# Kernel tuning notes

Measured on AMD Instinct MI355X. Metric: run time of the kernel, lower is better.

The kernel has to match this reference:

```python
import jax, jax.numpy as jnp
import numpy as np

T, D, DFF, E, K = 2048, 1024, 2816, 8, 2


def setup_inputs() -> dict:
    key = jax.random.key(0)
    k1, k2, k3, k4, k5, k6 = jax.random.split(key, 6)
    return {
        "x": jax.random.normal(k1, (T, D), dtype=jnp.float32),
        "topk_weight": jax.random.uniform(k2, (T, K), dtype=jnp.float32),
        "gate_w": jax.random.normal(k3, (E, DFF, D), dtype=jnp.float32) * 0.02,
        "up_w": jax.random.normal(k4, (E, DFF, D), dtype=jnp.float32) * 0.02,
        "down_w": jax.random.normal(k5, (E, D, DFF), dtype=jnp.float32) * 0.02,
        "topk_ids": jax.random.randint(k6, (T, K), 0, E, dtype=jnp.int64),
    }


def reference(x, topk_weight, gate_w, up_w, down_w, topk_ids):
    # x: [T, D]; topk_ids/topk_weight: [T, K]
    # Per expert: SwiGLU MLP over all tokens, combined with the per-token
    # routing weight for that expert (0 if the expert was not selected).
    out = jnp.zeros_like(x)
    num_experts = gate_w.shape[0]
    for e in range(num_experts):
        h = jax.nn.silu(x @ gate_w[e].T) * (x @ up_w[e].T)  # [T, DFF]
        y = h @ down_w[e].T                                  # [T, D]
        # sum over top-k slots of routing weight where this expert was chosen
        w_e = jnp.sum(jnp.where(topk_ids == e, topk_weight, 0.0), axis=1)  # [T]
        out = out + y * w_e[:, None]
    return out
```

## Files before the change

### kernel.cpp

```cpp
#include <hip/hip_runtime.h>
#include <stdint.h>

typedef __attribute__((ext_vector_type(8))) __bf16 bf16x8;
typedef __attribute__((ext_vector_type(4))) float f32x4;
typedef __attribute__((ext_vector_type(8))) unsigned short ushort8;

#define T_TOK 2048
#define D_DIM 1024
#define DFF   2816
#define NEXP  8
#define NROWS 4096
#define BK    32
#define NW_ELEM (NEXP * DFF * D_DIM)
#define MAXTM2 24

#define SWZ(r,g) ((g) ^ (((r) >> 1) & 3))

#define TL_N    0
#define TL_BASE 16
#define TL_VAL  80
#define TL_EXP  144

__device__ __forceinline__ void lds_cp16(const void* g, void* l) {
  __builtin_amdgcn_global_load_lds(
      (const __attribute__((address_space(1))) void*)g,
      (__attribute__((address_space(3))) void*)l, 16, 0, 0);
}

__device__ __forceinline__ ushort8 pack_bf16x8(float4 a, float4 b) {
  union { __bf16 h[8]; ushort8 u; } r;
  r.h[0] = (__bf16)a.x; r.h[1] = (__bf16)a.y; r.h[2] = (__bf16)a.z; r.h[3] = (__bf16)a.w;
  r.h[4] = (__bf16)b.x; r.h[5] = (__bf16)b.y; r.h[6] = (__bf16)b.z; r.h[7] = (__bf16)b.w;
  return r.u;
}

__device__ __forceinline__ unsigned short f2bf(float f) {
  union { __bf16 h; unsigned short u; } r;
  r.h = (__bf16)f;
  return r.u;
}

__device__ __forceinline__ float bf2f(unsigned short u) {
  union { uint32_t u; float f; } v; v.u = (uint32_t)u << 16;
  return v.f;
}

#define PIPE_BARRIER_VM3() do { \
    asm volatile("s_waitcnt vmcnt(3)" ::: "memory"); \
    __builtin_amdgcn_s_barrier(); \
  } while (0)

__global__ __launch_bounds__(512) void routing_kernel(
    const int* __restrict__ ids, const float* __restrict__ w,
    int* __restrict__ cnt, int* __restrict__ off,
    int* __restrict__ tok, float* __restrict__ wgt, int* __restrict__ rowmap,
    int* __restrict__ tl2)
{
  __shared__ int s_cnt[NEXP];
  __shared__ int s_off[NEXP];
  const int lane = threadIdx.x & 63;
  const int e    = threadIdx.x >> 6;

  int total = 0;
  for (int c = 0; c < NROWS / 64; ++c) {
    int id = ids[c * 64 + lane];
    unsigned long long b = __ballot(id == e);
    total += __popcll(b);
  }
  if (lane == 0) s_cnt[e] = total;
  __syncthreads();
  if (threadIdx.x == 0) {
    int acc = 0, n2 = 0;
    for (int i = 0; i < NEXP; ++i) {
      s_off[i] = acc; off[i] = acc; cnt[i] = s_cnt[i];
      for (int j = 0; j < s_cnt[i]; j += 256) {
        tl2[TL_BASE + n2] = acc + j;
        tl2[TL_VAL  + n2] = min(256, s_cnt[i] - j);
        tl2[TL_EXP  + n2] = i;
        ++n2;
      }
      acc += s_cnt[i];
    }
    tl2[TL_N] = n2;
  }
  __syncthreads();
  int base = s_off[e];
  for (int c = 0; c < NROWS / 64; ++c) {
    int idx = c * 64 + lane;
    int id = ids[idx];
    bool m = (id == e);
    unsigned long long b = __ballot(m);
    int pos = __popcll(b & ((1ull << lane) - 1ull));
    if (m) {
      tok[base + pos] = idx >> 1;
      wgt[base + pos] = w[idx];
      rowmap[idx] = base + pos;
    }
    base += __popcll(b);
  }
}

__global__ __launch_bounds__(256) void gather_x_kernel(
    const float* __restrict__ x, const int* __restrict__ tok,
    unsigned short* __restrict__ xg)
{
  const int i = blockIdx.x;
  const int t = tok[i];
  const float4 v = ((const float4*)(x + (size_t)t * D_DIM))[threadIdx.x];
  ushort4 o;
  o.x = f2bf(v.x); o.y = f2bf(v.y); o.z = f2bf(v.z); o.w = f2bf(v.w);
  ((ushort4*)(xg + (size_t)i * D_DIM))[threadIdx.x] = o;
}

__global__ __launch_bounds__(256) void wconv_gu_kernel(
    const float* __restrict__ gw, const float* __restrict__ uw,
    unsigned short* __restrict__ gb, unsigned short* __restrict__ ub)
{
  const size_t n = NW_ELEM / 8;
  const size_t stride = (size_t)gridDim.x * blockDim.x;
  for (size_t i = (size_t)blockIdx.x * blockDim.x + threadIdx.x;
       i < 2 * n; i += stride) {
    const bool up = (i >= n);
    const size_t idx = (up ? i - n : i) * 8;
    const float* src = up ? uw : gw;
    unsigned short* dst = up ? ub : gb;
    float4 a = *(const float4*)(src + idx);
    float4 b = *(const float4*)(src + idx + 4);
    *(ushort8*)(dst + idx) = pack_bf16x8(a, b);
  }
}

#define BM_A 256
#define BN_A 64
#define NT_A (DFF / BN_A)
#define NWORK_A (MAXTM2 * NT_A)
#define WCD_BLKS 1024
#define NWG_A (NWORK_A + WCD_BLKS)
#define KT_A (D_DIM / BK)

__global__ __launch_bounds__(512) void moe_gateup_bf(
    const unsigned short* __restrict__ gbuf, const unsigned short* __restrict__ ubuf,
    const unsigned short* __restrict__ xg, const float* __restrict__ wgt,
    const int* __restrict__ tl2,
    unsigned short* __restrict__ hbuf,
    const float* __restrict__ down_w, unsigned short* __restrict__ dbuf)
{
  const int bid = blockIdx.x;
  const int ntm = tl2[TL_N];
  const int nwork = ntm * NT_A;
  const int tid = threadIdx.x;
  if (bid >= nwork) {
    if (bid >= NWORK_A) {
      const int c = bid - NWORK_A;
      const size_t stride = (size_t)WCD_BLKS * 512;
      for (size_t i = (size_t)c * 512 + tid; i < NW_ELEM / 8; i += stride) {
        const size_t idx = i * 8;
        float4 a = *(const float4*)(down_w + idx);
        float4 b = *(const float4*)(down_w + idx + 4);
        *(ushort8*)(dbuf + idx) = pack_bf16x8(a, b);
      }
    }
    return;
  }
  const int tile = bid % ntm;
  const int nt   = bid / ntm;
  const int row_base = tl2[TL_BASE + tile];
  const int valid    = tl2[TL_VAL  + tile];
  const int e        = tl2[TL_EXP  + tile];
  const int n0 = nt * BN_A;

  __shared__ __align__(16) unsigned short Alds[3][BM_A * BK];
  __shared__ __align__(16) unsigned short Bg[3][BN_A * BK];
  __shared__ __align__(16) unsigned short Bu[3][BN_A * BK];

  const int lane = tid & 63;
  const int wid = tid >> 6;
  const int wm = wid >> 1, wn = wid & 1;
  const int lhi = lane >> 4, llo = lane & 15;

  f32x4 accg[4][2], accu[4][2];
  #pragma unroll
  for (int i = 0; i < 4; ++i)
    #pragma unroll
    for (int j = 0; j < 2; ++j) {
      accg[i][j] = (f32x4){0.f, 0.f, 0.f, 0.f};
      accu[i][j] = (f32x4){0.f, 0.f, 0.f, 0.f};
    }

  const unsigned short* gb = gbuf + ((size_t)e * DFF + n0) * D_DIM;
  const unsigned short* ub = ubuf + ((size_t)e * DFF + n0) * D_DIM;

  const int ar0 = tid >> 2, ag = tid & 3;
  const int ar1 = ar0 + 128;
  const size_t a_src0 = (size_t)(row_base + min(ar0, valid - 1)) * D_DIM + SWZ(ar0, ag) * 8;
  const size_t a_src1 = (size_t)(row_base + min(ar1, valid - 1)) * D_DIM + SWZ(ar1, ag) * 8;
  const int q = tid & 255;
  const int br = q >> 2, bg2 = q & 3;
  const size_t b_src = (size_t)br * D_DIM + SWZ(br, bg2) * 8;
  const unsigned short* bsrc_base = (tid < 256) ? gb : ub;
  unsigned short* bdst[3];
  bdst[0] = (tid < 256) ? &Bg[0][q * 8] : &Bu[0][q * 8];
  bdst[1] = (tid < 256) ? &Bg[1][q * 8] : &Bu[1][q * 8];
  bdst[2] = (tid < 256) ? &Bg[2][q * 8] : &Bu[2][q * 8];

  lds_cp16(xg + a_src0, &Alds[0][tid * 8]);
  lds_cp16(xg + a_src1, &Alds[0][(tid + 512) * 8]);
  lds_cp16(bsrc_base + b_src, bdst[0]);
  {
    const int k1 = BK;
    lds_cp16(xg + a_src0 + k1, &Alds[1][tid * 8]);
    lds_cp16(xg + a_src1 + k1, &Alds[1][(tid + 512) * 8]);
    lds_cp16(bsrc_base + b_src + k1, bdst[1]);
  }

  int cur = 0;
  for (int t = 0; t < KT_A; ++t) {
    PIPE_BARRIER_VM3();

    const int nb = (cur + 2 >= 3) ? cur - 1 : cur + 2;
    const int kn = (t + 2 < KT_A) ? (t + 2) * BK : 0;
    lds_cp16(xg + a_src0 + kn, &Alds[nb][tid * 8]);
    lds_cp16(xg + a_src1 + kn, &Alds[nb][(tid + 512) * 8]);
    lds_cp16(bsrc_base + b_src + kn, bdst[nb]);

    bf16x8 a[4], bgf[2], buf_[2];
    #pragma unroll
    for (int mi = 0; mi < 4; ++mi) {
      int row = wm * 64 + mi * 16 + llo;
      a[mi] = *(const bf16x8*)&Alds[cur][row * BK + SWZ(row, lhi) * 8];
    }
    #pragma unroll
    for (int ni = 0; ni < 2; ++ni) {
      int row = wn * 32 + ni * 16 + llo;
      bgf[ni]  = *(const bf16x8*)&Bg[cur][row * BK + SWZ(row, lhi) * 8];
      buf_[ni] = *(const bf16x8*)&Bu[cur][row * BK + SWZ(row, lhi) * 8];
    }
    #pragma unroll
    for (int mi = 0; mi < 4; ++mi)
      #pragma unroll
      for (int ni = 0; ni < 2; ++ni) {
        accg[mi][ni] = __builtin_amdgcn_mfma_f32_16x16x32_bf16(a[mi], bgf[ni], accg[mi][ni], 0, 0, 0);
        accu[mi][ni] = __builtin_amdgcn_mfma_f32_16x16x32_bf16(a[mi], buf_[ni], accu[mi][ni], 0, 0, 0);
      }

    cur = (cur + 1 >= 3) ? 0 : cur + 1;
  }

  #pragma unroll
  for (int mi = 0; mi < 4; ++mi) {
    #pragma unroll
    for (int r = 0; r < 4; ++r) {
      int row = wm * 64 + mi * 16 + lhi * 4 + r;
      if (row < valid) {
        int grow = row_base + row;
        float wv = wgt[grow];
        size_t base = (size_t)grow * DFF + n0 + wn * 32;
        #pragma unroll
        for (int ni = 0; ni < 2; ++ni) {
          float g = accg[mi][ni][r];
          float u = accu[mi][ni][r];
          float h = (g / (1.f + __expf(-g))) * u * wv;
          hbuf[base + ni * 16 + llo] = f2bf(h);
        }
      }
    }
  }
}

#define BM_B 256
#define BN_B 128
#define NT_B (D_DIM / BN_B)
#define SLICES_B 4
#define NWG_B (MAXTM2 * NT_B * SLICES_B)

template <bool USE_YBUF>
__global__ __launch_bounds__(512) void moe_down_bf(
    const unsigned short* __restrict__ dbuf,
    const unsigned short* __restrict__ hbuf,
    const int* __restrict__ tok,
    const int* __restrict__ tl2,
    unsigned short* __restrict__ ybuf, float* __restrict__ out_atomic)
{
  constexpr int KS = DFF / SLICES_B;
  constexpr int KT = KS / BK;

  const int bid = blockIdx.x;
  const int ntm = tl2[TL_N];
  const int nwork = ntm * NT_B * SLICES_B;
  if (bid >= nwork) return;
  const int tile = bid % ntm;
  const int r1_  = bid / ntm;
  const int nt = r1_ % NT_B;
  const int sl = r1_ / NT_B;
  const int row_base = tl2[TL_BASE + tile];
  const int valid    = tl2[TL_VAL  + tile];
  const int e        = tl2[TL_EXP  + tile];
  const int n0 = nt * BN_B;
  const int kbeg = sl * KS;

  __shared__ __align__(16) unsigned short Alds[3][BM_B * BK];
  __shared__ __align__(16) unsigned short Blds[3][BN_B * BK];

  const int tid = threadIdx.x, lane = tid & 63, wid = tid >> 6;
  const int wm = wid >> 1, wn = wid & 1;
  const int lhi = lane >> 4, llo = lane & 15;

  f32x4 acc[4][4];
  #pragma unroll
  for (int i = 0; i < 4; ++i)
    #pragma unroll
    for (int j = 0; j < 4; ++j) acc[i][j] = (f32x4){0.f, 0.f, 0.f, 0.f};

  const unsigned short* db = dbuf + ((size_t)e * D_DIM + n0) * DFF;

  const int ar0 = tid >> 2, ag = tid & 3;
  const int ar1 = ar0 + 128;
  const size_t a_src0 = (size_t)(row_base + min(ar0, valid - 1)) * DFF + SWZ(ar0, ag) * 8;
  const size_t a_src1 = (size_t)(row_base + min(ar1, valid - 1)) * DFF + SWZ(ar1, ag) * 8;
  const int brr = tid >> 2, bgg = tid & 3;
  const size_t b_src = (size_t)brr * DFF + SWZ(brr, bgg) * 8;

  lds_cp16(hbuf + a_src0 + kbeg, &Alds[0][tid * 8]);
  lds_cp16(hbuf + a_src1 + kbeg, &Alds[0][(tid + 512) * 8]);
  lds_cp16(db + b_src + kbeg, &Blds[0][tid * 8]);
  {
    const int k1 = kbeg + BK;
    lds_cp16(hbuf + a_src0 + k1, &Alds[1][tid * 8]);
    lds_cp16(hbuf + a_src1 + k1, &Alds[1][(tid + 512) * 8]);
    lds_cp16(db + b_src + k1, &Blds[1][tid * 8]);
  }

  int cur = 0;
  for (int t = 0; t < KT; ++t) {
    PIPE_BARRIER_VM3();

    const int nb = (cur + 2 >= 3) ? cur - 1 : cur + 2;
    const int kn = kbeg + ((t + 2 < KT) ? (t + 2) * BK : 0);
    lds_cp16(hbuf + a_src0 + kn, &Alds[nb][tid * 8]);
    lds_cp16(hbuf + a_src1 + kn, &Alds[nb][(tid + 512) * 8]);
    lds_cp16(db + b_src + kn, &Blds[nb][tid * 8]);

    bf16x8 a[4], b[4];
    #pragma unroll
    for (int mi = 0; mi < 4; ++mi) {
      int row = wm * 64 + mi * 16 + llo;
      a[mi] = *(const bf16x8*)&Alds[cur][row * BK + SWZ(row, lhi) * 8];
    }
    #pragma unroll
    for (int ni = 0; ni < 4; ++ni) {
      int row = wn * 64 + ni * 16 + llo;
      b[ni] = *(const bf16x8*)&Blds[cur][row * BK + SWZ(row, lhi) * 8];
    }
    #pragma unroll
    for (int mi = 0; mi < 4; ++mi)
      #pragma unroll
      for (int ni = 0; ni < 4; ++ni)
        acc[mi][ni] = __builtin_amdgcn_mfma_f32_16x16x32_bf16(a[mi], b[ni], acc[mi][ni], 0, 0, 0);

    cur = (cur + 1 >= 3) ? 0 : cur + 1;
  }

  #pragma unroll
  for (int mi = 0; mi < 4; ++mi) {
    #pragma unroll
    for (int r = 0; r < 4; ++r) {
      int row = wm * 64 + mi * 16 + lhi * 4 + r;
      if (row < valid) {
        if (USE_YBUF) {
          unsigned short* yp = ybuf + ((size_t)sl * NROWS + row_base + row) * D_DIM + n0 + wn * 64;
          #pragma unroll
          for (int ni = 0; ni < 4; ++ni) yp[ni * 16 + llo] = f2bf(acc[mi][ni][r]);
        } else {
          int tk = tok[row_base + row];
          float* op = out_atomic + (size_t)tk * D_DIM + n0 + wn * 64;
          #pragma unroll
          for (int ni = 0; ni < 4; ++ni) atomicAdd(op + ni * 16 + llo, acc[mi][ni][r]);
        }
      }
    }
  }
}

__global__ __launch_bounds__(256) void combine_kernel(
    const unsigned short* __restrict__ ybuf, const int* __restrict__ rowmap,
    float* __restrict__ out)
{
  const int t = blockIdx.x;
  const int d = threadIdx.x * 4;
  const int r0 = rowmap[t * 2], r1 = rowmap[t * 2 + 1];
  float s0 = 0.f, s1 = 0.f, s2 = 0.f, s3 = 0.f;
  #pragma unroll
  for (int sl = 0; sl < SLICES_B; ++sl) {
    ushort4 a = *(const ushort4*)(ybuf + ((size_t)sl * NROWS + r0) * D_DIM + d);
    ushort4 b = *(const ushort4*)(ybuf + ((size_t)sl * NROWS + r1) * D_DIM + d);
    s0 += bf2f(a.x) + bf2f(b.x);
    s1 += bf2f(a.y) + bf2f(b.y);
    s2 += bf2f(a.z) + bf2f(b.z);
    s3 += bf2f(a.w) + bf2f(b.w);
  }
  float4 s = {s0, s1, s2, s3};
  *(float4*)(out + (size_t)t * D_DIM + d) = s;
}

extern "C" void kernel_launch(void* const* d_in, const int* in_sizes, int n_in,
                              void* d_out, int out_size, void* d_ws, size_t ws_size,
                              hipStream_t stream) {
  const float* x      = (const float*)d_in[0];
  const float* topk_w = (const float*)d_in[1];
  const float* gate_w = (const float*)d_in[2];
  const float* up_w   = (const float*)d_in[3];
  const float* down_w = (const float*)d_in[4];
  const int*   ids    = (const int*)d_in[5];
  float* out = (float*)d_out;

  char* ws = (char*)d_ws;
  int*   cnt    = (int*)(ws + 0);
  int*   off    = (int*)(ws + 32);
  int*   tok    = (int*)(ws + 64);
  float* wgt    = (float*)(ws + 64 + NROWS * 4);
  int*   rowmap = (int*)(ws + 64 + NROWS * 8);
  int*   tl2    = (int*)(ws + 50688);

  const size_t XG_OFF = 65536;
  const size_t XG_SZ  = (size_t)NROWS * D_DIM * 2;
  const size_t HB_OFF = XG_OFF + XG_SZ;
  const size_t HB_SZ  = (size_t)NROWS * DFF * 2;
  const size_t W_SZ   = (size_t)NW_ELEM * 2;
  const size_t GB_OFF = HB_OFF + HB_SZ;
  const size_t UB_OFF = GB_OFF + W_SZ;
  const size_t DB_OFF = UB_OFF + W_SZ;
  const size_t YB_OFF = DB_OFF + W_SZ;
  const size_t YB_SZ  = (size_t)SLICES_B * NROWS * D_DIM * 2;

  unsigned short* xg   = (unsigned short*)(ws + XG_OFF);
  unsigned short* hbuf = (unsigned short*)(ws + HB_OFF);
  unsigned short* gbuf = (unsigned short*)(ws + GB_OFF);
  unsigned short* ubuf = (unsigned short*)(ws + UB_OFF);
  unsigned short* dbuf = (unsigned short*)(ws + DB_OFF);
  unsigned short* ybuf = (unsigned short*)(ws + YB_OFF);

  routing_kernel<<<1, 512, 0, stream>>>(ids, topk_w, cnt, off, tok, wgt, rowmap, tl2);
  gather_x_kernel<<<NROWS, 256, 0, stream>>>(x, tok, xg);
  wconv_gu_kernel<<<4096, 256, 0, stream>>>(gate_w, up_w, gbuf, ubuf);
  moe_gateup_bf<<<NWG_A, 512, 0, stream>>>(gbuf, ubuf, xg, wgt, tl2, hbuf, down_w, dbuf);

  if (ws_size >= YB_OFF + YB_SZ) {
    moe_down_bf<true><<<NWG_B, 512, 0, stream>>>(dbuf, hbuf, tok, tl2, ybuf, nullptr);
    combine_kernel<<<T_TOK, 256, 0, stream>>>(ybuf, rowmap, out);
  } else {
    hipMemsetAsync(d_out, 0, (size_t)out_size * sizeof(float), stream);
    moe_down_bf<false><<<NWG_B, 512, 0, stream>>>(dbuf, hbuf, tok, tl2, nullptr, out);
  }
}
```

Baseline: 242.3 us.

## Fuse gate/up weight conversion into panel-resident gate-up GEMM

Removes the separate fp32-to-bf16 conversion kernel for gate and up weights. Each block now loads a 32-column panel of gate and up weights straight from fp32, converts it into LDS once (about 128KB), and loops over all token tiles of its expert, streaming only activations through a double buffer. This avoids writing and re-reading bf16 weight copies in global memory. In exchange, LDS use per block is high, which limits occupancy, and the per-block panel load is not overlapped with compute.

```diff
diff --git a/kernel.cpp b/kernel.cpp
--- a/kernel.cpp
+++ b/kernel.cpp
@@ -44,11 +44,6 @@
   union { uint32_t u; float f; } v; v.u = (uint32_t)u << 16;
   return v.f;
 }
-
-#define PIPE_BARRIER_VM3() do { \
-    asm volatile("s_waitcnt vmcnt(3)" ::: "memory"); \
-    __builtin_amdgcn_s_barrier(); \
-  } while (0)
 
 __global__ __launch_bounds__(512) void routing_kernel(
     const int* __restrict__ ids, const float* __restrict__ w,
@@ -112,155 +107,131 @@
   ((ushort4*)(xg + (size_t)i * D_DIM))[threadIdx.x] = o;
 }
 
-__global__ __launch_bounds__(256) void wconv_gu_kernel(
-    const float* __restrict__ gw, const float* __restrict__ uw,
-    unsigned short* __restrict__ gb, unsigned short* __restrict__ ub)
-{
-  const size_t n = NW_ELEM / 8;
-  const size_t stride = (size_t)gridDim.x * blockDim.x;
-  for (size_t i = (size_t)blockIdx.x * blockDim.x + threadIdx.x;
-       i < 2 * n; i += stride) {
-    const bool up = (i >= n);
-    const size_t idx = (up ? i - n : i) * 8;
-    const float* src = up ? uw : gw;
-    unsigned short* dst = up ? ub : gb;
-    float4 a = *(const float4*)(src + idx);
-    float4 b = *(const float4*)(src + idx + 4);
-    *(ushort8*)(dst + idx) = pack_bf16x8(a, b);
-  }
-}
-
-#define BM_A 256
-#define BN_A 64
-#define NT_A (DFF / BN_A)
-#define NWORK_A (MAXTM2 * NT_A)
+#define BN_P 32
+#define NTP (DFF / BN_P)
+#define NWORK_P (NEXP * NTP)
 #define WCD_BLKS 1024
-#define NWG_A (NWORK_A + WCD_BLKS)
+#define NWG_P (NWORK_P + WCD_BLKS)
 #define KT_A (D_DIM / BK)
 
-__global__ __launch_bounds__(512) void moe_gateup_bf(
-    const unsigned short* __restrict__ gbuf, const unsigned short* __restrict__ ubuf,
+__global__ __launch_bounds__(512) void moe_gateup_panel(
+    const float* __restrict__ gate_w, const float* __restrict__ up_w,
     const unsigned short* __restrict__ xg, const float* __restrict__ wgt,
-    const int* __restrict__ tl2,
+    const int* __restrict__ cnt, const int* __restrict__ off,
     unsigned short* __restrict__ hbuf,
     const float* __restrict__ down_w, unsigned short* __restrict__ dbuf)
 {
   const int bid = blockIdx.x;
-  const int ntm = tl2[TL_N];
-  const int nwork = ntm * NT_A;
   const int tid = threadIdx.x;
-  if (bid >= nwork) {
-    if (bid >= NWORK_A) {
-      const int c = bid - NWORK_A;
-      const size_t stride = (size_t)WCD_BLKS * 512;
-      for (size_t i = (size_t)c * 512 + tid; i < NW_ELEM / 8; i += stride) {
-        const size_t idx = i * 8;
-        float4 a = *(const float4*)(down_w + idx);
-        float4 b = *(const float4*)(down_w + idx + 4);
-        *(ushort8*)(dbuf + idx) = pack_bf16x8(a, b);
-      }
+  if (bid >= NWORK_P) {
+    const int c = bid - NWORK_P;
+    const size_t stride = (size_t)WCD_BLKS * 512;
+    for (size_t i = (size_t)c * 512 + tid; i < NW_ELEM / 8; i += stride) {
+      const size_t idx = i * 8;
+      float4 a = *(const float4*)(down_w + idx);
+      float4 b = *(const float4*)(down_w + idx + 4);
+      *(ushort8*)(dbuf + idx) = pack_bf16x8(a, b);
     }
     return;
   }
-  const int tile = bid % ntm;
-  const int nt   = bid / ntm;
-  const int row_base = tl2[TL_BASE + tile];
-  const int valid    = tl2[TL_VAL  + tile];
-  const int e        = tl2[TL_EXP  + tile];
-  const int n0 = nt * BN_A;
-
-  __shared__ __align__(16) unsigned short Alds[3][BM_A * BK];
-  __shared__ __align__(16) unsigned short Bg[3][BN_A * BK];
-  __shared__ __align__(16) unsigned short Bu[3][BN_A * BK];
-
-  const int lane = tid & 63;
-  const int wid = tid >> 6;
-  const int wm = wid >> 1, wn = wid & 1;
+  const int e  = bid / NTP;
+  const int nt = bid % NTP;
+  const int cnte = cnt[e];
+  if (cnte == 0) return;
+  const int off_e = off[e];
+  const int n0 = nt * BN_P;
+
+  __shared__ __align__(16) unsigned short Bg[BN_P * D_DIM];
+  __shared__ __align__(16) unsigned short Bu[BN_P * D_DIM];
+  __shared__ __align__(16) unsigned short Alds[2][256 * BK];
+
+  {
+    const float* gp = gate_w + ((size_t)e * DFF + n0) * D_DIM;
+    const float* up = up_w   + ((size_t)e * DFF + n0) * D_DIM;
+    #pragma unroll
+    for (int it = 0; it < (BN_P * D_DIM / 8) / 512; ++it) {
+      const int c = it * 512 + tid;
+      const int r = c >> 7, g = c & 127;
+      const int dst = r * D_DIM + ((g ^ (r & 7)) * 8);
+      const float* s1 = gp + (size_t)r * D_DIM + g * 8;
+      *(ushort8*)&Bg[dst] = pack_bf16x8(*(const float4*)s1, *(const float4*)(s1 + 4));
+      const float* s2 = up + (size_t)r * D_DIM + g * 8;
+      *(ushort8*)&Bu[dst] = pack_bf16x8(*(const float4*)s2, *(const float4*)(s2 + 4));
+    }
+  }
+  __syncthreads();
+
+  const int lane = tid & 63, wid = tid >> 6;
   const int lhi = lane >> 4, llo = lane & 15;
-
-  f32x4 accg[4][2], accu[4][2];
-  #pragma unroll
-  for (int i = 0; i < 4; ++i)
-    #pragma unroll
-    for (int j = 0; j < 2; ++j) {
-      accg[i][j] = (f32x4){0.f, 0.f, 0.f, 0.f};
-      accu[i][j] = (f32x4){0.f, 0.f, 0.f, 0.f};
-    }
-
-  const unsigned short* gb = gbuf + ((size_t)e * DFF + n0) * D_DIM;
-  const unsigned short* ub = ubuf + ((size_t)e * DFF + n0) * D_DIM;
-
   const int ar0 = tid >> 2, ag = tid & 3;
   const int ar1 = ar0 + 128;
-  const size_t a_src0 = (size_t)(row_base + min(ar0, valid - 1)) * D_DIM + SWZ(ar0, ag) * 8;
-  const size_t a_src1 = (size_t)(row_base + min(ar1, valid - 1)) * D_DIM + SWZ(ar1, ag) * 8;
-  const int q = tid & 255;
-  const int br = q >> 2, bg2 = q & 3;
-  const size_t b_src = (size_t)br * D_DIM + SWZ(br, bg2) * 8;
-  const unsigned short* bsrc_base = (tid < 256) ? gb : ub;
-  unsigned short* bdst[3];
-  bdst[0] = (tid < 256) ? &Bg[0][q * 8] : &Bu[0][q * 8];
-  bdst[1] = (tid < 256) ? &Bg[1][q * 8] : &Bu[1][q * 8];
-  bdst[2] = (tid < 256) ? &Bg[2][q * 8] : &Bu[2][q * 8];
-
-  lds_cp16(xg + a_src0, &Alds[0][tid * 8]);
-  lds_cp16(xg + a_src1, &Alds[0][(tid + 512) * 8]);
-  lds_cp16(bsrc_base + b_src, bdst[0]);
-  {
-    const int k1 = BK;
-    lds_cp16(xg + a_src0 + k1, &Alds[1][tid * 8]);
-    lds_cp16(xg + a_src1 + k1, &Alds[1][(tid + 512) * 8]);
-    lds_cp16(bsrc_base + b_src + k1, bdst[1]);
-  }
-
-  int cur = 0;
-  for (int t = 0; t < KT_A; ++t) {
-    PIPE_BARRIER_VM3();
-
-    const int nb = (cur + 2 >= 3) ? cur - 1 : cur + 2;
-    const int kn = (t + 2 < KT_A) ? (t + 2) * BK : 0;
-    lds_cp16(xg + a_src0 + kn, &Alds[nb][tid * 8]);
-    lds_cp16(xg + a_src1 + kn, &Alds[nb][(tid + 512) * 8]);
-    lds_cp16(bsrc_base + b_src + kn, bdst[nb]);
-
-    bf16x8 a[4], bgf[2], buf_[2];
-    #pragma unroll
-    for (int mi = 0; mi < 4; ++mi) {
-      int row = wm * 64 + mi * 16 + llo;
-      a[mi] = *(const bf16x8*)&Alds[cur][row * BK + SWZ(row, lhi) * 8];
-    }
-    #pragma unroll
-    for (int ni = 0; ni < 2; ++ni) {
-      int row = wn * 32 + ni * 16 + llo;
-      bgf[ni]  = *(const bf16x8*)&Bg[cur][row * BK + SWZ(row, lhi) * 8];
-      buf_[ni] = *(const bf16x8*)&Bu[cur][row * BK + SWZ(row, lhi) * 8];
-    }
-    #pragma unroll
-    for (int mi = 0; mi < 4; ++mi)
+
+  const int nmt = (cnte + 255) >> 8;
+  for (int mt = 0; mt < nmt; ++mt) {
+    const int row_base = off_e + (mt << 8);
+    const int valid = min(256, cnte - (mt << 8));
+    const size_t a_src0 = (size_t)(row_base + min(ar0, valid - 1)) * D_DIM + SWZ(ar0, ag) * 8;
+    const size_t a_src1 = (size_t)(row_base + min(ar1, valid - 1)) * D_DIM + SWZ(ar1, ag) * 8;
+
+    f32x4 accg[2][2], accu[2][2];
+    #pragma unroll
+    for (int i = 0; i < 2; ++i)
+      #pragma unroll
+      for (int j = 0; j < 2; ++j) {
+        accg[i][j] = (f32x4){0.f, 0.f, 0.f, 0.f};
+        accu[i][j] = (f32x4){0.f, 0.f, 0.f, 0.f};
+      }
+
+    lds_cp16(xg + a_src0, &Alds[0][tid * 8]);
+    lds_cp16(xg + a_src1, &Alds[0][(tid + 512) * 8]);
+
+    for (int t = 0; t < KT_A; ++t) {
+      __builtin_amdgcn_s_barrier();
+      const int kn = (t + 1 < KT_A) ? (t + 1) * BK : 0;
+      lds_cp16(xg + a_src0 + kn, &Alds[(t + 1) & 1][tid * 8]);
+      lds_cp16(xg + a_src1 + kn, &Alds[(t + 1) & 1][(tid + 512) * 8]);
+      asm volatile("s_waitcnt vmcnt(2)" ::: "memory");
+      __builtin_amdgcn_s_barrier();
+
+      bf16x8 a[2], bgf[2], buf_[2];
+      #pragma unroll
+      for (int mi = 0; mi < 2; ++mi) {
+        int row = wid * 32 + mi * 16 + llo;
+        a[mi] = *(const bf16x8*)&Alds[t & 1][row * BK + SWZ(row, lhi) * 8];
+      }
       #pragma unroll
       for (int ni = 0; ni < 2; ++ni) {
-        accg[mi][ni] = __builtin_amdgcn_mfma_f32_16x16x32_bf16(a[mi], bgf[ni], accg[mi][ni], 0, 0, 0);
-        accu[mi][ni] = __builtin_amdgcn_mfma_f32_16x16x32_bf16(a[mi], buf_[ni], accu[mi][ni], 0, 0, 0);
-      }
-
-    cur = (cur + 1 >= 3) ? 0 : cur + 1;
-  }
-
-  #pragma unroll
-  for (int mi = 0; mi < 4; ++mi) {
-    #pragma unroll
-    for (int r = 0; r < 4; ++r) {
-      int row = wm * 64 + mi * 16 + lhi * 4 + r;
-      if (row < valid) {
-        int grow = row_base + row;
-        float wv = wgt[grow];
-        size_t base = (size_t)grow * DFF + n0 + wn * 32;
+        int rn = ni * 16 + llo;
+        int gk = t * 4 + lhi;
+        int eo = rn * D_DIM + ((gk ^ (rn & 7)) * 8);
+        bgf[ni]  = *(const bf16x8*)&Bg[eo];
+        buf_[ni] = *(const bf16x8*)&Bu[eo];
+      }
+      #pragma unroll
+      for (int mi = 0; mi < 2; ++mi)
         #pragma unroll
         for (int ni = 0; ni < 2; ++ni) {
-          float g = accg[mi][ni][r];
-          float u = accu[mi][ni][r];
-          float h = (g / (1.f + __expf(-g))) * u * wv;
-          hbuf[base + ni * 16 + llo] = f2bf(h);
+          accg[mi][ni] = __builtin_amdgcn_mfma_f32_16x16x32_bf16(a[mi], bgf[ni], accg[mi][ni], 0, 0, 0);
+          accu[mi][ni] = __builtin_amdgcn_mfma_f32_16x16x32_bf16(a[mi], buf_[ni], accu[mi][ni], 0, 0, 0);
+        }
+    }
+
+    #pragma unroll
+    for (int mi = 0; mi < 2; ++mi) {
+      #pragma unroll
+      for (int r_ = 0; r_ < 4; ++r_) {
+        int row = wid * 32 + mi * 16 + lhi * 4 + r_;
+        if (row < valid) {
+          int grow = row_base + row;
+          float wv = wgt[grow];
+          size_t base = (size_t)grow * DFF + n0;
+          #pragma unroll
+          for (int ni = 0; ni < 2; ++ni) {
+            float g = accg[mi][ni][r_];
+            float u = accu[mi][ni][r_];
+            float h = (g / (1.f + __expf(-g))) * u * wv;
+            hbuf[base + ni * 16 + llo] = f2bf(h);
+          }
         }
       }
     }
@@ -272,6 +243,11 @@
 #define NT_B (D_DIM / BN_B)
 #define SLICES_B 4
 #define NWG_B (MAXTM2 * NT_B * SLICES_B)
+
+#define PIPE_BARRIER_VM3() do { \
+    asm volatile("s_waitcnt vmcnt(3)" ::: "memory"); \
+    __builtin_amdgcn_s_barrier(); \
+  } while (0)
 
 template <bool USE_YBUF>
 __global__ __launch_bounds__(512) void moe_down_bf(
@@ -426,23 +402,19 @@
   const size_t HB_OFF = XG_OFF + XG_SZ;
   const size_t HB_SZ  = (size_t)NROWS * DFF * 2;
   const size_t W_SZ   = (size_t)NW_ELEM * 2;
-  const size_t GB_OFF = HB_OFF + HB_SZ;
-  const size_t UB_OFF = GB_OFF + W_SZ;
-  const size_t DB_OFF = UB_OFF + W_SZ;
+  const size_t DB_OFF = HB_OFF + HB_SZ;
   const size_t YB_OFF = DB_OFF + W_SZ;
   const size_t YB_SZ  = (size_t)SLICES_B * NROWS * D_DIM * 2;
 
   unsigned short* xg   = (unsigned short*)(ws + XG_OFF);
   unsigned short* hbuf = (unsigned short*)(ws + HB_OFF);
-  unsigned short* gbuf = (unsigned short*)(ws + GB_OFF);
-  unsigned short* ubuf = (unsigned short*)(ws + UB_OFF);
   unsigned short* dbuf = (unsigned short*)(ws + DB_OFF);
   unsigned short* ybuf = (unsigned short*)(ws + YB_OFF);
 
   routing_kernel<<<1, 512, 0, stream>>>(ids, topk_w, cnt, off, tok, wgt, rowmap, tl2);
   gather_x_kernel<<<NROWS, 256, 0, stream>>>(x, tok, xg);
-  wconv_gu_kernel<<<4096, 256, 0, stream>>>(gate_w, up_w, gbuf, ubuf);
-  moe_gateup_bf<<<NWG_A, 512, 0, stream>>>(gbuf, ubuf, xg, wgt, tl2, hbuf, down_w, dbuf);
+  moe_gateup_panel<<<NWG_P, 512, 0, stream>>>(gate_w, up_w, xg, wgt, cnt, off,
+                                              hbuf, down_w, dbuf);
 
   if (ws_size >= YB_OFF + YB_SZ) {
     moe_down_bf<true><<<NWG_B, 512, 0, stream>>>(dbuf, hbuf, tok, tl2, ybuf, nullptr);
```

Result: slower. 277.7 us (+14.6%).

## Switch MoE GEMMs to 32x32x16 MFMA and shrink gate-up blocks to 256 threads

Applied to the files above, without the earlier changes.

Both the gate/up and down GEMM kernels now use 32x32x16 bf16 MFMA tiles with 16-float accumulators instead of 16x16x32 tiles, cutting the number of MFMA issues and LDS fragment loads per tile. The gate/up kernel drops to 256 threads (4 waves each covering 64 rows by all 64 columns). Each thread issues more async loads per stage, so the wait count goes to vmcnt(6). The down-weight conversion loop in the spare blocks is rescaled to match. This trades higher per-wave register pressure and fewer waves per block for denser matrix-core work.

```diff
diff --git a/kernel.cpp b/kernel.cpp
--- a/kernel.cpp
+++ b/kernel.cpp
@@ -2,7 +2,7 @@
 #include <stdint.h>
 
 typedef __attribute__((ext_vector_type(8))) __bf16 bf16x8;
-typedef __attribute__((ext_vector_type(4))) float f32x4;
+typedef __attribute__((ext_vector_type(16))) float f32x16;
 typedef __attribute__((ext_vector_type(8))) unsigned short ushort8;
 
 #define T_TOK 2048
@@ -44,11 +44,6 @@
   union { uint32_t u; float f; } v; v.u = (uint32_t)u << 16;
   return v.f;
 }
-
-#define PIPE_BARRIER_VM3() do { \
-    asm volatile("s_waitcnt vmcnt(3)" ::: "memory"); \
-    __builtin_amdgcn_s_barrier(); \
-  } while (0)
 
 __global__ __launch_bounds__(512) void routing_kernel(
     const int* __restrict__ ids, const float* __restrict__ w,
@@ -138,7 +133,7 @@
 #define NWG_A (NWORK_A + WCD_BLKS)
 #define KT_A (D_DIM / BK)
 
-__global__ __launch_bounds__(512) void moe_gateup_bf(
+__global__ __launch_bounds__(256) void moe_gateup_bf(
     const unsigned short* __restrict__ gbuf, const unsigned short* __restrict__ ubuf,
     const unsigned short* __restrict__ xg, const float* __restrict__ wgt,
     const int* __restrict__ tl2,
@@ -152,8 +147,8 @@
   if (bid >= nwork) {
     if (bid >= NWORK_A) {
       const int c = bid - NWORK_A;
-      const size_t stride = (size_t)WCD_BLKS * 512;
-      for (size_t i = (size_t)c * 512 + tid; i < NW_ELEM / 8; i += stride) {
+      const size_t stride = (size_t)WCD_BLKS * 256;
+      for (size_t i = (size_t)c * 256 + tid; i < NW_ELEM / 8; i += stride) {
         const size_t idx = i * 8;
         float4 a = *(const float4*)(down_w + idx);
         float4 b = *(const float4*)(down_w + idx + 4);
@@ -175,92 +170,91 @@
 
   const int lane = tid & 63;
   const int wid = tid >> 6;
-  const int wm = wid >> 1, wn = wid & 1;
-  const int lhi = lane >> 4, llo = lane & 15;
-
-  f32x4 accg[4][2], accu[4][2];
-  #pragma unroll
-  for (int i = 0; i < 4; ++i)
+  const int l31 = lane & 31, lhi5 = lane >> 5;
+
+  f32x16 accg[2][2], accu[2][2];
+  #pragma unroll
+  for (int i = 0; i < 2; ++i)
     #pragma unroll
     for (int j = 0; j < 2; ++j) {
-      accg[i][j] = (f32x4){0.f, 0.f, 0.f, 0.f};
-      accu[i][j] = (f32x4){0.f, 0.f, 0.f, 0.f};
+      #pragma unroll
+      for (int r = 0; r < 16; ++r) { accg[i][j][r] = 0.f; accu[i][j][r] = 0.f; }
     }
 
   const unsigned short* gb = gbuf + ((size_t)e * DFF + n0) * D_DIM;
   const unsigned short* ub = ubuf + ((size_t)e * DFF + n0) * D_DIM;
 
-  const int ar0 = tid >> 2, ag = tid & 3;
-  const int ar1 = ar0 + 128;
-  const size_t a_src0 = (size_t)(row_base + min(ar0, valid - 1)) * D_DIM + SWZ(ar0, ag) * 8;
-  const size_t a_src1 = (size_t)(row_base + min(ar1, valid - 1)) * D_DIM + SWZ(ar1, ag) * 8;
-  const int q = tid & 255;
-  const int br = q >> 2, bg2 = q & 3;
-  const size_t b_src = (size_t)br * D_DIM + SWZ(br, bg2) * 8;
-  const unsigned short* bsrc_base = (tid < 256) ? gb : ub;
-  unsigned short* bdst[3];
-  bdst[0] = (tid < 256) ? &Bg[0][q * 8] : &Bu[0][q * 8];
-  bdst[1] = (tid < 256) ? &Bg[1][q * 8] : &Bu[1][q * 8];
-  bdst[2] = (tid < 256) ? &Bg[2][q * 8] : &Bu[2][q * 8];
-
-  lds_cp16(xg + a_src0, &Alds[0][tid * 8]);
-  lds_cp16(xg + a_src1, &Alds[0][(tid + 512) * 8]);
-  lds_cp16(bsrc_base + b_src, bdst[0]);
-  {
-    const int k1 = BK;
-    lds_cp16(xg + a_src0 + k1, &Alds[1][tid * 8]);
-    lds_cp16(xg + a_src1 + k1, &Alds[1][(tid + 512) * 8]);
-    lds_cp16(bsrc_base + b_src + k1, bdst[1]);
-  }
+  uint32_t a_off[4];
+  #pragma unroll
+  for (int j = 0; j < 4; ++j) {
+    int ar = (tid + j * 256) >> 2;
+    a_off[j] = (uint32_t)((row_base + min(ar, valid - 1)) * D_DIM + SWZ(ar, tid & 3) * 8);
+  }
+  const int brr = tid >> 2;
+  const uint32_t b_off = (uint32_t)(brr * D_DIM + SWZ(brr, tid & 3) * 8);
+
+  #pragma unroll
+  for (int j = 0; j < 4; ++j) lds_cp16(xg + a_off[j], &Alds[0][(tid + j * 256) * 8]);
+  lds_cp16(gb + b_off, &Bg[0][tid * 8]);
+  lds_cp16(ub + b_off, &Bu[0][tid * 8]);
+  #pragma unroll
+  for (int j = 0; j < 4; ++j) lds_cp16(xg + a_off[j] + BK, &Alds[1][(tid + j * 256) * 8]);
+  lds_cp16(gb + b_off + BK, &Bg[1][tid * 8]);
+  lds_cp16(ub + b_off + BK, &Bu[1][tid * 8]);
 
   int cur = 0;
   for (int t = 0; t < KT_A; ++t) {
-    PIPE_BARRIER_VM3();
+    asm volatile("s_waitcnt vmcnt(6)" ::: "memory");
+    __builtin_amdgcn_s_barrier();
 
     const int nb = (cur + 2 >= 3) ? cur - 1 : cur + 2;
     const int kn = (t + 2 < KT_A) ? (t + 2) * BK : 0;
-    lds_cp16(xg + a_src0 + kn, &Alds[nb][tid * 8]);
-    lds_cp16(xg + a_src1 + kn, &Alds[nb][(tid + 512) * 8]);
-    lds_cp16(bsrc_base + b_src + kn, bdst[nb]);
-
-    bf16x8 a[4], bgf[2], buf_[2];
-    #pragma unroll
-    for (int mi = 0; mi < 4; ++mi) {
-      int row = wm * 64 + mi * 16 + llo;
-      a[mi] = *(const bf16x8*)&Alds[cur][row * BK + SWZ(row, lhi) * 8];
-    }
-    #pragma unroll
-    for (int ni = 0; ni < 2; ++ni) {
-      int row = wn * 32 + ni * 16 + llo;
-      bgf[ni]  = *(const bf16x8*)&Bg[cur][row * BK + SWZ(row, lhi) * 8];
-      buf_[ni] = *(const bf16x8*)&Bu[cur][row * BK + SWZ(row, lhi) * 8];
-    }
-    #pragma unroll
-    for (int mi = 0; mi < 4; ++mi)
-      #pragma unroll
-      for (int ni = 0; ni < 2; ++ni) {
-        accg[mi][ni] = __builtin_amdgcn_mfma_f32_16x16x32_bf16(a[mi], bgf[ni], accg[mi][ni], 0, 0, 0);
-        accu[mi][ni] = __builtin_amdgcn_mfma_f32_16x16x32_bf16(a[mi], buf_[ni], accu[mi][ni], 0, 0, 0);
-      }
-
+    #pragma unroll
+    for (int j = 0; j < 4; ++j) lds_cp16(xg + a_off[j] + kn, &Alds[nb][(tid + j * 256) * 8]);
+    lds_cp16(gb + b_off + kn, &Bg[nb][tid * 8]);
+    lds_cp16(ub + b_off + kn, &Bu[nb][tid * 8]);
+
+    #pragma unroll
+    for (int ks = 0; ks < 2; ++ks) {
+      const int gidx = ks * 2 + lhi5;
+      bf16x8 a[2], bgf[2], buf_[2];
+      #pragma unroll
+      for (int mi = 0; mi < 2; ++mi) {
+        int row = wid * 64 + mi * 32 + l31;
+        a[mi] = *(const bf16x8*)&Alds[cur][row * BK + SWZ(row, gidx) * 8];
+      }
+      #pragma unroll
+      for (int ci = 0; ci < 2; ++ci) {
+        int rb = ci * 32 + l31;
+        bgf[ci]  = *(const bf16x8*)&Bg[cur][rb * BK + SWZ(rb, gidx) * 8];
+        buf_[ci] = *(const bf16x8*)&Bu[cur][rb * BK + SWZ(rb, gidx) * 8];
+      }
+      #pragma unroll
+      for (int mi = 0; mi < 2; ++mi)
+        #pragma unroll
+        for (int ci = 0; ci < 2; ++ci) {
+          accg[mi][ci] = __builtin_amdgcn_mfma_f32_32x32x16_bf16(a[mi], bgf[ci], accg[mi][ci], 0, 0, 0);
+          accu[mi][ci] = __builtin_amdgcn_mfma_f32_32x32x16_bf16(a[mi], buf_[ci], accu[mi][ci], 0, 0, 0);
+        }
+    }
     cur = (cur + 1 >= 3) ? 0 : cur + 1;
   }
 
   #pragma unroll
-  for (int mi = 0; mi < 4; ++mi) {
-    #pragma unroll
-    for (int r = 0; r < 4; ++r) {
-      int row = wm * 64 + mi * 16 + lhi * 4 + r;
+  for (int mi = 0; mi < 2; ++mi) {
+    #pragma unroll
+    for (int r = 0; r < 16; ++r) {
+      int row = wid * 64 + mi * 32 + (r & 3) + 8 * (r >> 2) + 4 * lhi5;
       if (row < valid) {
         int grow = row_base + row;
         float wv = wgt[grow];
-        size_t base = (size_t)grow * DFF + n0 + wn * 32;
+        size_t base = (size_t)grow * DFF + n0;
         #pragma unroll
-        for (int ni = 0; ni < 2; ++ni) {
-          float g = accg[mi][ni][r];
-          float u = accu[mi][ni][r];
+        for (int ci = 0; ci < 2; ++ci) {
+          float g = accg[mi][ci][r];
+          float u = accu[mi][ci][r];
           float h = (g / (1.f + __expf(-g))) * u * wv;
-          hbuf[base + ni * 16 + llo] = f2bf(h);
+          hbuf[base + ci * 32 + l31] = f2bf(h);
         }
       }
     }
@@ -272,6 +266,11 @@
 #define NT_B (D_DIM / BN_B)
 #define SLICES_B 4
 #define NWG_B (MAXTM2 * NT_B * SLICES_B)
+
+#define PIPE_BARRIER_VM3() do { \
+    asm volatile("s_waitcnt vmcnt(3)" ::: "memory"); \
+    __builtin_amdgcn_s_barrier(); \
+  } while (0)
 
 template <bool USE_YBUF>
 __global__ __launch_bounds__(512) void moe_down_bf(
@@ -303,13 +302,15 @@
 
   const int tid = threadIdx.x, lane = tid & 63, wid = tid >> 6;
   const int wm = wid >> 1, wn = wid & 1;
-  const int lhi = lane >> 4, llo = lane & 15;
-
-  f32x4 acc[4][4];
-  #pragma unroll
-  for (int i = 0; i < 4; ++i)
-    #pragma unroll
-    for (int j = 0; j < 4; ++j) acc[i][j] = (f32x4){0.f, 0.f, 0.f, 0.f};
+  const int l31 = lane & 31, lhi5 = lane >> 5;
+
+  f32x16 acc[2][2];
+  #pragma unroll
+  for (int i = 0; i < 2; ++i)
+    #pragma unroll
+    for (int j = 0; j < 2; ++j)
+      #pragma unroll
+      for (int r = 0; r < 16; ++r) acc[i][j][r] = 0.f;
 
   const unsigned short* db = dbuf + ((size_t)e * D_DIM + n0) * DFF;
 
@@ -340,41 +341,44 @@
     lds_cp16(hbuf + a_src1 + kn, &Alds[nb][(tid + 512) * 8]);
     lds_cp16(db + b_src + kn, &Blds[nb][tid * 8]);
 
-    bf16x8 a[4], b[4];
-    #pragma unroll
-    for (int mi = 0; mi < 4; ++mi) {
-      int row = wm * 64 + mi * 16 + llo;
-      a[mi] = *(const bf16x8*)&Alds[cur][row * BK + SWZ(row, lhi) * 8];
-    }
-    #pragma unroll
-    for (int ni = 0; ni < 4; ++ni) {
-      int row = wn * 64 + ni * 16 + llo;
-      b[ni] = *(const bf16x8*)&Blds[cur][row * BK + SWZ(row, lhi) * 8];
-    }
-    #pragma unroll
-    for (int mi = 0; mi < 4; ++mi)
-      #pragma unroll
-      for (int ni = 0; ni < 4; ++ni)
-        acc[mi][ni] = __builtin_amdgcn_mfma_f32_16x16x32_bf16(a[mi], b[ni], acc[mi][ni], 0, 0, 0);
-
+    #pragma unroll
+    for (int ks = 0; ks < 2; ++ks) {
+      const int gidx = ks * 2 + lhi5;
+      bf16x8 a[2], b[2];
+      #pragma unroll
+      for (int mi = 0; mi < 2; ++mi) {
+        int row = wm * 64 + mi * 32 + l31;
+        a[mi] = *(const bf16x8*)&Alds[cur][row * BK + SWZ(row, gidx) * 8];
+      }
+      #pragma unroll
+      for (int ci = 0; ci < 2; ++ci) {
+        int rb = wn * 64 + ci * 32 + l31;
+        b[ci] = *(const bf16x8*)&Blds[cur][rb * BK + SWZ(rb, gidx) * 8];
+      }
+      #pragma unroll
+      for (int mi = 0; mi < 2; ++mi)
+        #pragma unroll
+        for (int ci = 0; ci < 2; ++ci)
+          acc[mi][ci] = __builtin_amdgcn_mfma_f32_32x32x16_bf16(a[mi], b[ci], acc[mi][ci], 0, 0, 0);
+    }
     cur = (cur + 1 >= 3) ? 0 : cur + 1;
   }
 
   #pragma unroll
-  for (int mi = 0; mi < 4; ++mi) {
-    #pragma unroll
-    for (int r = 0; r < 4; ++r) {
-      int row = wm * 64 + mi * 16 + lhi * 4 + r;
+  for (int mi = 0; mi < 2; ++mi) {
+    #pragma unroll
+    for (int r = 0; r < 16; ++r) {
+      int row = wm * 64 + mi * 32 + (r & 3) + 8 * (r >> 2) + 4 * lhi5;
       if (row < valid) {
         if (USE_YBUF) {
           unsigned short* yp = ybuf + ((size_t)sl * NROWS + row_base + row) * D_DIM + n0 + wn * 64;
           #pragma unroll
-          for (int ni = 0; ni < 4; ++ni) yp[ni * 16 + llo] = f2bf(acc[mi][ni][r]);
+          for (int ci = 0; ci < 2; ++ci) yp[ci * 32 + l31] = f2bf(acc[mi][ci][r]);
         } else {
           int tk = tok[row_base + row];
           float* op = out_atomic + (size_t)tk * D_DIM + n0 + wn * 64;
           #pragma unroll
-          for (int ni = 0; ni < 4; ++ni) atomicAdd(op + ni * 16 + llo, acc[mi][ni][r]);
+          for (int ci = 0; ci < 2; ++ci) atomicAdd(op + ci * 32 + l31, acc[mi][ci][r]);
         }
       }
     }
@@ -442,7 +446,7 @@
   routing_kernel<<<1, 512, 0, stream>>>(ids, topk_w, cnt, off, tok, wgt, rowmap, tl2);
   gather_x_kernel<<<NROWS, 256, 0, stream>>>(x, tok, xg);
   wconv_gu_kernel<<<4096, 256, 0, stream>>>(gate_w, up_w, gbuf, ubuf);
-  moe_gateup_bf<<<NWG_A, 512, 0, stream>>>(gbuf, ubuf, xg, wgt, tl2, hbuf, down_w, dbuf);
+  moe_gateup_bf<<<NWG_A, 256, 0, stream>>>(gbuf, ubuf, xg, wgt, tl2, hbuf, down_w, dbuf);
 
   if (ws_size >= YB_OFF + YB_SZ) {
     moe_down_bf<true><<<NWG_B, 512, 0, stream>>>(dbuf, hbuf, tok, tl2, ybuf, nullptr);
```

Result: slower. 321.1 us (+32.5%).
